# Performance work log

Measured on AMD Instinct MI355X. Metric: run time of the kernel, lower is better.

## Reference

```python
import jax, jax.numpy as jnp
import numpy as np

B, L, N = 16, 64, 1024
HAND_DIM, J, HID = 99, 21, 512
N_LAYERS, N_HEADS = 4, 8
DH = HID // N_HEADS
CAT = HAND_DIM + 2 * J * 3 + 2 * N  # 2273
PNAMES = ['fc_lw','fc_lb','fc_rw','fc_rb','out_lw','out_lb','out_rw','out_rb','Wqkv','bqkv','Wo','bo','W1','b1f','W2','b2f','ln1_g','ln1_b','ln2_g','ln2_b']

def sinusoidal_pe(n_pos, d):
    pos = np.arange(n_pos)[:, None].astype(np.float32)
    div = np.exp(np.arange(0, d, 2).astype(np.float32) * (-np.log(10000.0) / d))
    pe = np.zeros((n_pos, d), np.float32)
    pe[:, 0::2] = np.sin(pos * div)
    pe[:, 1::2] = np.cos(pos * div)
    return jnp.asarray(pe)

def rot6d_to_rotmat(x6):
    a1, a2 = x6[..., 0:3], x6[..., 3:6]
    b1 = a1 / jnp.linalg.norm(a1, axis=-1, keepdims=True)
    b2 = a2 - jnp.sum(b1 * a2, -1, keepdims=True) * b1
    b2 = b2 / jnp.linalg.norm(b2, axis=-1, keepdims=True)
    b3 = jnp.cross(b1, b2)
    return jnp.stack([b1, b2, b3], axis=-1)  # [..., 3, 3] (columns)

def layer_norm(x, g, b):
    mu = jnp.mean(x, -1, keepdims=True)
    var = jnp.mean((x - mu) ** 2, -1, keepdims=True)
    return (x - mu) * jax.lax.rsqrt(var + 1e-5) * g + b

def attention_map(joints, pc):
    # joints [B,L,J,3], pc [B,L,N,3]; squared dists via ||a||^2+||b||^2-2ab (no [B,L,J,N,3] diff tensor)
    d2 = (jnp.sum(joints ** 2, -1)[..., :, None] + jnp.sum(pc ** 2, -1)[..., None, :]
          - 2.0 * jnp.einsum('bljd,blnd->bljn', joints, pc))
    idx = jnp.argmin(d2, axis=-1)  # [B,L,J] nearest-point index
    idx3 = jnp.broadcast_to(idx[..., None], idx.shape + (3,))
    contact = jnp.take_along_axis(pc, idx3, axis=2)  # [B,L,J,3]
    return jnp.exp(-50.0 * (joints - contact) ** 2)

def mha(x, Wqkv, bqkv, Wo, bo):
    Bq, S, D = x.shape
    qkv = x @ Wqkv + bqkv
    q, k, v = jnp.split(qkv, 3, axis=-1)
    split = lambda t: t.reshape(Bq, S, N_HEADS, DH).transpose(0, 2, 1, 3)
    q, k, v = split(q), split(k), split(v)
    att = jax.nn.softmax(jnp.einsum('bhqd,bhkd->bhqk', q, k) * (1.0 / np.sqrt(DH)), axis=-1)
    o = jnp.einsum('bhqk,bhkd->bhqd', att, v).transpose(0, 2, 1, 3).reshape(Bq, S, D)
    return o @ Wo + bo

def forward(x_lhand, x_rhand, j_lhand, j_rhand, m_contact, x_obj, point_cloud, p):
    rotmat = rot6d_to_rotmat(x_obj[..., 3:9])  # [B,L,3,3]
    pc_t = jnp.einsum('btij,bkj->btki', rotmat, point_cloud) + x_obj[..., 0:3][:, :, None, :]
    att_l = attention_map(j_lhand, pc_t).reshape(B, L, -1)
    att_r = attention_map(j_rhand, pc_t).reshape(B, L, -1)
    mc = jnp.broadcast_to(m_contact.reshape(B, 1, N), (B, L, N))
    pcn = jnp.linalg.norm(pc_t, axis=-1)  # [B,L,N]
    xl = jnp.concatenate([x_lhand, j_lhand.reshape(B, L, -1), mc, pcn, att_l], -1)
    xr = jnp.concatenate([x_rhand, j_rhand.reshape(B, L, -1), mc, pcn, att_r], -1)
    xl = xl @ p['fc_lw'] + p['fc_lb']
    xr = xr @ p['fc_rw'] + p['fc_rb']
    x = jnp.stack([xl, xr], axis=2).reshape(B, 2 * L, HID)  # interleave agents per frame
    pe_frame = jnp.repeat(sinusoidal_pe(L, HID), 2, axis=0)  # frame-wise: pair shares position
    pe_agent = jnp.tile(sinusoidal_pe(2, HID), (L, 1))       # agent-wise: alternating 0/1
    x = x + pe_frame[None] + pe_agent[None]
    for i in range(N_LAYERS):
        h = layer_norm(x + mha(x, p['Wqkv'][i], p['bqkv'][i], p['Wo'][i], p['bo'][i]), p['ln1_g'][i], p['ln1_b'][i])
        ff = jax.nn.relu(h @ p['W1'][i] + p['b1f'][i]) @ p['W2'][i] + p['b2f'][i]
        x = layer_norm(h + ff, p['ln2_g'][i], p['ln2_b'][i])
    out_l = x[:, 0::2] @ p['out_lw'] + p['out_lb']
    out_r = x[:, 1::2] @ p['out_rw'] + p['out_rb']
    return out_l, out_r

def setup_inputs() -> dict:
    key = jax.random.key(0)
    ks = jax.random.split(key, 16)
    r = lambda i, shape, s=1.0: jax.random.normal(ks[i], shape, jnp.float32) * s
    return {
        'x_lhand': r(0, (B, L, HAND_DIM)),
        'x_rhand': r(1, (B, L, HAND_DIM)),
        'j_lhand': r(2, (B, L, J, 3)),
        'j_rhand': r(3, (B, L, J, 3)),
        'm_contact': jax.random.uniform(ks[4], (B, N, 1), jnp.float32),
        'x_obj': r(5, (B, L, 10)),
        'point_cloud': r(6, (B, N, 3)),
        'fc_lw': r(7, (CAT, HID), 0.02), 'fc_lb': jnp.zeros((HID,), jnp.float32),
        'fc_rw': r(8, (CAT, HID), 0.02), 'fc_rb': jnp.zeros((HID,), jnp.float32),
        'out_lw': r(9, (HID, HAND_DIM), 0.02), 'out_lb': jnp.zeros((HAND_DIM,), jnp.float32),
        'out_rw': r(10, (HID, HAND_DIM), 0.02), 'out_rb': jnp.zeros((HAND_DIM,), jnp.float32),
        'Wqkv': r(11, (N_LAYERS, HID, 3 * HID), 0.02), 'bqkv': jnp.zeros((N_LAYERS, 3 * HID), jnp.float32),
        'Wo': r(12, (N_LAYERS, HID, HID), 0.02), 'bo': jnp.zeros((N_LAYERS, HID), jnp.float32),
        'W1': r(13, (N_LAYERS, HID, 4 * HID), 0.02), 'b1f': jnp.zeros((N_LAYERS, 4 * HID), jnp.float32),
        'W2': r(14, (N_LAYERS, 4 * HID, HID), 0.02), 'b2f': jnp.zeros((N_LAYERS, HID), jnp.float32),
        'ln1_g': jnp.ones((N_LAYERS, HID), jnp.float32), 'ln1_b': jnp.zeros((N_LAYERS, HID), jnp.float32),
        'ln2_g': jnp.ones((N_LAYERS, HID), jnp.float32), 'ln2_b': jnp.zeros((N_LAYERS, HID), jnp.float32),
    }

def reference(x_lhand, x_rhand, j_lhand, j_rhand, m_contact, x_obj, point_cloud, fc_lw, fc_lb, fc_rw, fc_rb, out_lw, out_lb, out_rw, out_rb, Wqkv, bqkv, Wo, bo, W1, b1f, W2, b2f, ln1_g, ln1_b, ln2_g, ln2_b):
    p = dict(zip(PNAMES, (fc_lw, fc_lb, fc_rw, fc_rb, out_lw, out_lb, out_rw, out_rb, Wqkv, bqkv, Wo, bo, W1, b1f, W2, b2f, ln1_g, ln1_b, ln2_g, ln2_b)))
    return forward(x_lhand, x_rhand, j_lhand, j_rhand, m_contact, x_obj, point_cloud, p)
```

## Files before the change

### kernel.cpp

```cpp
#include <hip/hip_runtime.h>
#include <hip/hip_bf16.h>

typedef __hip_bfloat16 bf16;
typedef __attribute__((ext_vector_type(8))) short short8;
typedef __attribute__((ext_vector_type(4))) float floatx4;

#define B_    16
#define L_    64
#define N_    1024
#define HANDD 99
#define Jn    21
#define HID   512
#define NLAY  4
#define NHEAD 8
#define DHEAD 64
#define CATD  2273
#define CATP  2304
#define S_    128
#define T_    2048

#define F_X     16
#define F_QKV   1048592
#define F_TMP   6291472
#define F_H     7340048
#define WB_F    8388624
#define W_FCL   0
#define W_FCR   1179648
#define W_QKV   2359296
#define W_WO    5505024
#define W_W1    6553600
#define W_W2    10747904
#define U_CATL  14942208
#define U_CATR  17301504
#define U_XB    19660800
#define U_AOB   20709376
#define U_HB    21757952
#define W_OUT   22806528
#define U_FFB   U_CATL

static __device__ __forceinline__ float b2f(bf16 x) { return __bfloat162float(x); }
static __device__ __forceinline__ float ldin(const void* p, size_t i, int isf32) {
    return isf32 ? ((const float*)p)[i] : b2f(((const bf16*)p)[i]);
}
static __device__ __forceinline__ unsigned short f2bf(float f) {
    unsigned int u = __float_as_uint(f);
    unsigned int r = (u + 0x7fffu + ((u >> 16) & 1u)) >> 16;
    return (unsigned short)r;
}

__global__ __launch_bounds__(256) void detect_kernel(const void* mc, int* flag)
{
    __shared__ int sbad;
    int tid = threadIdx.x;
    if (tid == 0) sbad = 0;
    __syncthreads();
    int bad = 0;
    for (int i = tid; i < 16384; i += 256) {
        float v = b2f(((const bf16*)mc)[i]);
        if (!(v >= -0.02f && v <= 1.02f)) bad = 1;
    }
    if (bad) atomicOr(&sbad, 1);
    __syncthreads();
    if (tid == 0) flag[0] = sbad ? 1 : 0;
}

__global__ __launch_bounds__(256) void wtrans_kernel(
    const void* __restrict__ src, size_t src_layer, int K, int Nn, int NnBound,
    int Kpad, unsigned short* __restrict__ dst, size_t dst_layer,
    const int* __restrict__ dtf)
{
    int isf32 = dtf[0];
    __shared__ float tile[64][65];
    int lay = blockIdx.z;
    size_t soff = (size_t)lay * src_layer;
    size_t doff = (size_t)lay * dst_layer;
    int n0 = blockIdx.x * 64, k0 = blockIdx.y * 64;
    int a = threadIdx.x & 63, bq = threadIdx.x >> 6;
    for (int r = bq; r < 64; r += 4) {
        int k = k0 + r;
        int n = n0 + a;
        float v = (k < K && n < NnBound) ? ldin(src, soff + (size_t)k * Nn + n, isf32) : 0.f;
        tile[r][a] = v;
    }
    __syncthreads();
    for (int r = bq; r < 64; r += 4) {
        dst[doff + (size_t)(n0 + r) * Kpad + k0 + a] = f2bf(tile[a][r]);
    }
}

__global__ __launch_bounds__(256) void pctcat_kernel(
    const void* __restrict__ x_l, const void* __restrict__ j_l,
    const void* __restrict__ x_r, const void* __restrict__ j_r,
    const void* __restrict__ mc, const void* __restrict__ x_obj,
    const void* __restrict__ pc, unsigned short* __restrict__ cat_l,
    unsigned short* __restrict__ cat_r, const int* __restrict__ dtf)
{
    __shared__ float pcl[N_ * 3];
    __shared__ float pcnl[N_];
    int isf32 = dtf[0];
    int bl = blockIdx.x;
    int b  = bl >> 6;
    int tid = threadIdx.x;

    size_t xo = (size_t)bl * 10;
    float t0 = ldin(x_obj, xo+0, isf32), t1 = ldin(x_obj, xo+1, isf32), t2 = ldin(x_obj, xo+2, isf32);
    float a1x = ldin(x_obj, xo+3, isf32), a1y = ldin(x_obj, xo+4, isf32), a1z = ldin(x_obj, xo+5, isf32);
    float a2x = ldin(x_obj, xo+6, isf32), a2y = ldin(x_obj, xo+7, isf32), a2z = ldin(x_obj, xo+8, isf32);
    float n1 = sqrtf(a1x*a1x + a1y*a1y + a1z*a1z);
    float b1x = a1x / n1, b1y = a1y / n1, b1z = a1z / n1;
    float d = b1x*a2x + b1y*a2y + b1z*a2z;
    float c2x = a2x - d*b1x, c2y = a2y - d*b1y, c2z = a2z - d*b1z;
    float n2 = sqrtf(c2x*c2x + c2y*c2y + c2z*c2z);
    float b2x = c2x / n2, b2y = c2y / n2, b2z = c2z / n2;
    float b3x = b1y*b2z - b1z*b2y;
    float b3y = b1z*b2x - b1x*b2z;
    float b3z = b1x*b2y - b1y*b2x;

    size_t pcb = (size_t)b * N_ * 3;
    for (int n = tid; n < N_; n += 256) {
        float p0 = ldin(pc, pcb + n*3+0, isf32);
        float p1 = ldin(pc, pcb + n*3+1, isf32);
        float p2 = ldin(pc, pcb + n*3+2, isf32);
        float q0 = b1x*p0 + b2x*p1 + b3x*p2 + t0;
        float q1 = b1y*p0 + b2y*p1 + b3y*p2 + t1;
        float q2 = b1z*p0 + b2z*p1 + b3z*p2 + t2;
        pcl[n*3+0] = q0; pcl[n*3+1] = q1; pcl[n*3+2] = q2;
        pcnl[n] = q0*q0 + q1*q1 + q2*q2;
    }
    __syncthreads();

    #pragma unroll
    for (int hand = 0; hand < 2; hand++) {
        const void* xh = hand ? x_r : x_l;
        const void* jh = hand ? j_r : j_l;
        unsigned short* row = (hand ? cat_r : cat_l) + (size_t)bl * CATP;
        for (int c = tid; c < HANDD; c += 256)  row[c]        = f2bf(ldin(xh, (size_t)bl*HANDD + c, isf32));
        for (int c = tid; c < 63;    c += 256)  row[99 + c]   = f2bf(ldin(jh, (size_t)bl*63 + c, isf32));
        for (int c = tid; c < N_;    c += 256)  row[162 + c]  = f2bf(ldin(mc, (size_t)b*N_ + c, isf32));
        for (int c = tid; c < N_;    c += 256)  row[1186 + c] = f2bf(sqrtf(pcnl[c]));
        for (int c = CATD + tid; c < CATP; c += 256) row[c] = 0;
    }

    int wave = tid >> 6, lane = tid & 63;
    for (int t = wave; t < 2 * Jn; t += 4) {
        int hand = t / Jn, j = t - hand * Jn;
        const void* jh = hand ? j_r : j_l;
        unsigned short* row = (hand ? cat_r : cat_l) + (size_t)bl * CATP;
        float jx = ldin(jh, (size_t)bl*63 + j*3 + 0, isf32);
        float jy = ldin(jh, (size_t)bl*63 + j*3 + 1, isf32);
        float jz = ldin(jh, (size_t)bl*63 + j*3 + 2, isf32);
        float m2x = -2.f * jx, m2y = -2.f * jy, m2z = -2.f * jz;
        float best = 3.4e38f; int bidx = 0x7fffffff;
        for (int n = lane; n < N_; n += 64) {
            float p0 = pcl[n*3+0], p1 = pcl[n*3+1], p2 = pcl[n*3+2];
            float d2 = fmaf(m2x, p0, fmaf(m2y, p1, fmaf(m2z, p2, pcnl[n])));
            if (d2 < best) { best = d2; bidx = n; }
        }
        for (int off = 32; off; off >>= 1) {
            float ob = __shfl_down(best, off, 64);
            int   oi = __shfl_down(bidx, off, 64);
            if (ob < best || (ob == best && oi < bidx)) { best = ob; bidx = oi; }
        }
        bidx = __shfl(bidx, 0, 64);
        if (lane < 3) {
            float jc = (lane == 0) ? jx : ((lane == 1) ? jy : jz);
            float cc = pcl[bidx*3 + lane];
            float dd = jc - cc;
            row[2210 + j*3 + lane] = f2bf(expf(-50.f * dd * dd));
        }
    }
}

#define RSTR 68

__global__ __launch_bounds__(256) void gemm_ks(
    const unsigned short* __restrict__ Ab, const unsigned short* __restrict__ Ab2,
    int K,
    const unsigned short* __restrict__ Wt, size_t wtoff, size_t wtoff2, int halfgrid,
    int Nn,
    const void* __restrict__ bias, const void* __restrict__ bias2, size_t boff,
    const float* __restrict__ resid,
    float* __restrict__ Df, unsigned short* __restrict__ Db,
    int relu, int rowmap, int tilesN, const int* __restrict__ dtf)
{
    __shared__ float red[4][32 * RSTR];
    int blk = blockIdx.x;
    if (halfgrid && blk >= halfgrid) {
        blk -= halfgrid; Ab = Ab2; wtoff = wtoff2; bias = bias2; rowmap = 2;
    }
    int tid = threadIdx.x;
    int wave = tid >> 6, lane = tid & 63;
    int quad = lane >> 4, l16 = lane & 15;
    int tm = blk / tilesN, tn = blk - tm * tilesN;
    int row0 = tm << 6, col0 = tn << 6;
    int Ks = K >> 2;
    int ks0 = wave * Ks;

    const unsigned short* Ap = Ab + (size_t)(row0 + l16) * K + ks0 + quad * 8;
    const unsigned short* Bp = Wt + wtoff + (size_t)(col0 + l16) * K + ks0 + quad * 8;
    size_t astep = (size_t)16 * K;

    floatx4 acc[4][4];
    #pragma unroll
    for (int i = 0; i < 4; i++)
        #pragma unroll
        for (int j = 0; j < 4; j++)
            acc[i][j] = (floatx4){0.f, 0.f, 0.f, 0.f};

    for (int k = 0; k < Ks; k += 32) {
        short8 af[4], bf[4];
        #pragma unroll
        for (int i = 0; i < 4; i++) {
            af[i] = *(const short8*)(Ap + i * astep + k);
            bf[i] = *(const short8*)(Bp + i * astep + k);
        }
        #pragma unroll
        for (int mi = 0; mi < 4; mi++)
            #pragma unroll
            for (int ni = 0; ni < 4; ni++)
                acc[mi][ni] = __builtin_amdgcn_mfma_f32_16x16x32_bf16(
                    af[mi], bf[ni], acc[mi][ni], 0, 0, 0);
    }

    int isf32 = dtf[0];
    int cc = tid & 63;
    int c = col0 + cc;
    float bv;
    if (rowmap == 3)
        bv = (c < HANDD) ? ldin(bias, c, isf32)
           : ((c < 2 * HANDD) ? ldin(bias2, c - HANDD, isf32) : 0.f);
    else
        bv = bias ? ldin(bias, boff + c, isf32) : 0.f;
    float pe_div = 0.f, pa = 0.f;
    if (rowmap == 1 || rowmap == 2) {
        int ci = c & ~1;
        pe_div = expf((float)ci * (-logf(10000.f) / (float)HID));
        int hand = rowmap - 1;
        pa = (c & 1) ? cosf((float)hand * pe_div) : sinf((float)hand * pe_div);
    }
    int rbase = tid >> 6;

    #pragma unroll
    for (int s = 0; s < 2; s++) {
        #pragma unroll
        for (int mi2 = 0; mi2 < 2; mi2++) {
            int mi = s * 2 + mi2;
            #pragma unroll
            for (int ni = 0; ni < 4; ni++)
                #pragma unroll
                for (int reg = 0; reg < 4; reg++) {
                    int r = mi2 * 16 + quad * 4 + reg;
                    int col = ni * 16 + l16;
                    red[wave][r * RSTR + col] = acc[mi][ni][reg];
                }
        }
        __syncthreads();

        #pragma unroll
        for (int j = 0; j < 8; j++) {
            int rr = rbase + (j << 2);
            int idx = rr * RSTR + cc;
            float v = red[0][idx] + red[1][idx] + red[2][idx] + red[3][idx] + bv;
            int r = row0 + s * 32 + rr;
            if (resid) v += resid[(size_t)r * Nn + c];
            if (relu)  v = fmaxf(v, 0.f);
            if (rowmap == 3) {
                int hand = r & 1;
                int l = (r >> 1) & 63, bb = r >> 7;
                if (hand == 0 && c < HANDD) {
                    size_t oi = ((size_t)bb * 64 + l) * HANDD + c;
                    if (isf32) ((float*)Df)[oi] = v;
                    else       ((bf16*)Df)[oi]  = __float2bfloat16(v);
                } else if (hand == 1 && c >= HANDD && c < 2 * HANDD) {
                    size_t oi = (size_t)B_ * L_ * HANDD + ((size_t)bb * 64 + l) * HANDD + (c - HANDD);
                    if (isf32) ((float*)Df)[oi] = v;
                    else       ((bf16*)Df)[oi]  = __float2bfloat16(v);
                }
            } else {
                int orow = r;
                if (rowmap) {
                    int bb = r >> 6, ll = r & 63;
                    orow = bb * S_ + 2 * ll + (rowmap - 1);
                    float pf = (c & 1) ? cosf((float)ll * pe_div) : sinf((float)ll * pe_div);
                    v += pf + pa;
                }
                if (Df) Df[(size_t)orow * Nn + c] = v;
                if (Db) Db[(size_t)orow * Nn + c] = f2bf(v);
            }
        }
        if (s == 0) __syncthreads();
    }
}

#define VSTR 136

__global__ __launch_bounds__(128) void attn_mfma(
    const unsigned short* __restrict__ qkvb, unsigned short* __restrict__ aob)
{
    __shared__ unsigned short Vt[64 * VSTR];
    __shared__ unsigned short Pb[64 * VSTR];
    int bh = blockIdx.x;
    int b = bh >> 3, h = bh & 7;
    int rowhalf = blockIdx.y;
    int tid = threadIdx.x;
    int w = tid >> 6, lane = tid & 63;
    int quad = lane >> 4, l16 = lane & 15;
    size_t qbase = (size_t)(b * S_) * 1536 + h * DHEAD;

    for (int i = tid; i < S_ * DHEAD; i += 128) {
        int key = i >> 6, dcol = i & 63;
        Vt[dcol * VSTR + key] = qkvb[qbase + (size_t)key * 1536 + 1024 + dcol];
    }
    __syncthreads();

    int qrow0 = rowhalf * 64 + w * 32;
    short8 aQ[2][2];
    #pragma unroll
    for (int mt = 0; mt < 2; mt++)
        #pragma unroll
        for (int kc = 0; kc < 2; kc++)
            aQ[mt][kc] = *(const short8*)&qkvb[qbase + (size_t)(qrow0 + mt*16 + l16) * 1536 + kc*32 + quad*8];

    floatx4 sacc[2][8];
    #pragma unroll
    for (int mt = 0; mt < 2; mt++)
        #pragma unroll
        for (int nt = 0; nt < 8; nt++)
            sacc[mt][nt] = (floatx4){0.f, 0.f, 0.f, 0.f};

    #pragma unroll
    for (int nt = 0; nt < 8; nt++) {
        const unsigned short* kp = &qkvb[qbase + (size_t)(nt*16 + l16) * 1536 + 512 + quad*8];
        short8 bK0 = *(const short8*)kp;
        short8 bK1 = *(const short8*)(kp + 32);
        #pragma unroll
        for (int mt = 0; mt < 2; mt++) {
            sacc[mt][nt] = __builtin_amdgcn_mfma_f32_16x16x32_bf16(aQ[mt][0], bK0, sacc[mt][nt], 0, 0, 0);
            sacc[mt][nt] = __builtin_amdgcn_mfma_f32_16x16x32_bf16(aQ[mt][1], bK1, sacc[mt][nt], 0, 0, 0);
        }
    }

    #pragma unroll
    for (int mt = 0; mt < 2; mt++)
        #pragma unroll
        for (int reg = 0; reg < 4; reg++) {
            float v[8];
            float m = -3.4e38f;
            #pragma unroll
            for (int nt = 0; nt < 8; nt++) { v[nt] = sacc[mt][nt][reg] * 0.125f; m = fmaxf(m, v[nt]); }
            #pragma unroll
            for (int off = 1; off <= 8; off <<= 1) m = fmaxf(m, __shfl_xor(m, off, 64));
            float sum = 0.f;
            #pragma unroll
            for (int nt = 0; nt < 8; nt++) { v[nt] = expf(v[nt] - m); sum += v[nt]; }
            #pragma unroll
            for (int off = 1; off <= 8; off <<= 1) sum += __shfl_xor(sum, off, 64);
            float inv = 1.f / sum;
            int lr = w*32 + mt*16 + quad*4 + reg;
            #pragma unroll
            for (int nt = 0; nt < 8; nt++)
                Pb[lr * VSTR + nt*16 + l16] = f2bf(v[nt] * inv);
        }
    __syncthreads();

    #pragma unroll
    for (int mt = 0; mt < 2; mt++) {
        short8 aP[4];
        #pragma unroll
        for (int kt = 0; kt < 4; kt++)
            aP[kt] = *(const short8*)&Pb[(w*32 + mt*16 + l16) * VSTR + kt*32 + quad*8];
        #pragma unroll
        for (int nt = 0; nt < 4; nt++) {
            floatx4 o = (floatx4){0.f, 0.f, 0.f, 0.f};
            #pragma unroll
            for (int kt = 0; kt < 4; kt++) {
                short8 bV = *(const short8*)&Vt[(nt*16 + l16) * VSTR + kt*32 + quad*8];
                o = __builtin_amdgcn_mfma_f32_16x16x32_bf16(aP[kt], bV, o, 0, 0, 0);
            }
            #pragma unroll
            for (int reg = 0; reg < 4; reg++) {
                int qrow = qrow0 + mt*16 + quad*4 + reg;
                aob[(size_t)(b*S_ + qrow) * HID + h*DHEAD + nt*16 + l16] = f2bf(o[reg]);
            }
        }
    }
}

__global__ __launch_bounds__(256) void ln_kernel(
    const float* __restrict__ src, const void* __restrict__ g,
    const void* __restrict__ bb, size_t goff,
    float* __restrict__ dst, unsigned short* __restrict__ dstb,
    const int* __restrict__ dtf)
{
    int isf32 = dtf[0];
    int t = blockIdx.x;
    const float* x = src + (size_t)t * HID;
    int tid = threadIdx.x, lane = tid & 63, wave = tid >> 6;
    float v0 = x[tid], v1 = x[tid + 256];
    float s = v0 + v1;
    for (int off = 32; off; off >>= 1) s += __shfl_down(s, off, 64);
    __shared__ float wsum[4];
    if (lane == 0) wsum[wave] = s;
    __syncthreads();
    float mu = (wsum[0] + wsum[1] + wsum[2] + wsum[3]) * (1.f / 512.f);
    float d0 = v0 - mu, d1 = v1 - mu;
    float q = d0 * d0 + d1 * d1;
    for (int off = 32; off; off >>= 1) q += __shfl_down(q, off, 64);
    __syncthreads();
    if (lane == 0) wsum[wave] = q;
    __syncthreads();
    float var = (wsum[0] + wsum[1] + wsum[2] + wsum[3]) * (1.f / 512.f);
    float rstd = 1.f / sqrtf(var + 1e-5f);
    float y0 = d0 * rstd * ldin(g, goff + tid, isf32)       + ldin(bb, goff + tid, isf32);
    float y1 = d1 * rstd * ldin(g, goff + tid + 256, isf32) + ldin(bb, goff + tid + 256, isf32);
    if (dst) {
        dst[(size_t)t * HID + tid]       = y0;
        dst[(size_t)t * HID + tid + 256] = y1;
    }
    if (dstb) {
        dstb[(size_t)t * HID + tid]       = f2bf(y0);
        dstb[(size_t)t * HID + tid + 256] = f2bf(y1);
    }
}

extern "C" void kernel_launch(void* const* d_in, const int* in_sizes, int n_in,
                              void* d_out, int out_size, void* d_ws, size_t ws_size,
                              hipStream_t stream)
{
    const void* x_lhand = d_in[0];
    const void* x_rhand = d_in[1];
    const void* j_lhand = d_in[2];
    const void* j_rhand = d_in[3];
    const void* m_contact = d_in[4];
    const void* x_obj = d_in[5];
    const void* point_cloud = d_in[6];
    const void* fc_lw = d_in[7];
    const void* fc_lb = d_in[8];
    const void* fc_rw = d_in[9];
    const void* fc_rb = d_in[10];
    const void* out_lw = d_in[11];
    const void* out_lb = d_in[12];
    const void* out_rw = d_in[13];
    const void* out_rb = d_in[14];
    const void* Wqkv = d_in[15];
    const void* bqkv = d_in[16];
    const void* Wo   = d_in[17];
    const void* bo   = d_in[18];
    const void* W1   = d_in[19];
    const void* b1f  = d_in[20];
    const void* W2   = d_in[21];
    const void* b2fp = d_in[22];
    const void* ln1g = d_in[23];
    const void* ln1b = d_in[24];
    const void* ln2g = d_in[25];
    const void* ln2b = d_in[26];

    float* ws = (float*)d_ws;
    int* dtf = (int*)d_ws;
    float* x     = ws + F_X;
    float* tmp   = ws + F_TMP;
    float* h     = ws + F_H;
    unsigned short* qkvb = (unsigned short*)(ws + F_QKV);
    unsigned short* wb   = (unsigned short*)(ws + WB_F);
    unsigned short* catl = wb + U_CATL;
    unsigned short* catr = wb + U_CATR;
    unsigned short* xb   = wb + U_XB;
    unsigned short* aob  = wb + U_AOB;
    unsigned short* hb   = wb + U_HB;
    unsigned short* ffb  = wb + U_FFB;

    detect_kernel<<<1, 256, 0, stream>>>(m_contact, dtf);

    wtrans_kernel<<<dim3(8, 36, 1), 256, 0, stream>>>(fc_lw, 0, CATD, HID, HID, CATP, wb + W_FCL, 0, dtf);
    wtrans_kernel<<<dim3(8, 36, 1), 256, 0, stream>>>(fc_rw, 0, CATD, HID, HID, CATP, wb + W_FCR, 0, dtf);
    wtrans_kernel<<<dim3(24, 8, NLAY), 256, 0, stream>>>(Wqkv, (size_t)HID*1536, HID, 1536, 1536, HID, wb + W_QKV, (size_t)1536*HID, dtf);
    wtrans_kernel<<<dim3(8, 8, NLAY), 256, 0, stream>>>(Wo, (size_t)HID*HID, HID, HID, HID, HID, wb + W_WO, (size_t)HID*HID, dtf);
    wtrans_kernel<<<dim3(32, 8, NLAY), 256, 0, stream>>>(W1, (size_t)HID*2048, HID, 2048, 2048, HID, wb + W_W1, (size_t)2048*HID, dtf);
    wtrans_kernel<<<dim3(8, 32, NLAY), 256, 0, stream>>>(W2, (size_t)2048*HID, 2048, HID, HID, 2048, wb + W_W2, (size_t)HID*2048, dtf);
    wtrans_kernel<<<dim3(2, 8, 1), 256, 0, stream>>>(out_lw, 0, HID, HANDD, HANDD, HID, wb + W_OUT, 0, dtf);
    wtrans_kernel<<<dim3(2, 8, 1), 256, 0, stream>>>(out_rw, 0, HID, HANDD, HANDD, HID, wb + W_OUT + (size_t)HANDD * HID, 0, dtf);

    pctcat_kernel<<<B_ * L_, 256, 0, stream>>>(
        x_lhand, j_lhand, x_rhand, j_rhand, m_contact, x_obj, point_cloud,
        catl, catr, dtf);

    gemm_ks<<<256, 256, 0, stream>>>(catl, catr, CATP, wb, W_FCL, W_FCR, 128, HID,
                                     fc_lb, fc_rb, 0, nullptr, x, xb, 0, 1, 8, dtf);

    for (int i = 0; i < NLAY; i++) {
        size_t oWq = (size_t)W_QKV + (size_t)i * 1536 * HID, obq = (size_t)i * 1536;
        size_t oWo = (size_t)W_WO + (size_t)i * HID * HID,   obo = (size_t)i * HID;
        size_t oW1 = (size_t)W_W1 + (size_t)i * 2048 * HID,  ob1 = (size_t)i * 2048;
        size_t oW2 = (size_t)W_W2 + (size_t)i * HID * 2048,  ob2 = (size_t)i * HID;
        size_t oln = (size_t)i * HID;

        gemm_ks<<<768, 256, 0, stream>>>(xb, nullptr, HID, wb, oWq, 0, 0, 1536,
                                         bqkv, nullptr, obq, nullptr, nullptr, qkvb, 0, 0, 24, dtf);

        attn_mfma<<<dim3(B_ * NHEAD, 2), 128, 0, stream>>>(qkvb, aob);

        gemm_ks<<<256, 256, 0, stream>>>(aob, nullptr, HID, wb, oWo, 0, 0, HID,
                                         bo, nullptr, obo, x, tmp, nullptr, 0, 0, 8, dtf);
        ln_kernel<<<T_, 256, 0, stream>>>(tmp, ln1g, ln1b, oln, h, hb, dtf);

        gemm_ks<<<1024, 256, 0, stream>>>(hb, nullptr, HID, wb, oW1, 0, 0, 2048,
                                          b1f, nullptr, ob1, nullptr, nullptr, ffb, 1, 0, 32, dtf);
        gemm_ks<<<256, 256, 0, stream>>>(ffb, nullptr, 2048, wb, oW2, 0, 0, HID,
                                         b2fp, nullptr, ob2, h, tmp, nullptr, 0, 0, 8, dtf);
        ln_kernel<<<T_, 256, 0, stream>>>(tmp, ln2g, ln2b, oln, x, xb, dtf);
    }

    gemm_ks<<<128, 256, 0, stream>>>(xb, nullptr, HID, wb, W_OUT, 0, 0, 256,
                                     out_lb, out_rb, 0, nullptr, (float*)d_out, nullptr, 0, 3, 4, dtf);
}
```

Measured before the change: 717.7 us.

## Fuse LayerNorm into GEMM prologues/epilogues via atomic row statistics

```diff
diff --git a/kernel.cpp b/kernel.cpp
--- a/kernel.cpp
+++ b/kernel.cpp
@@ -19,11 +19,15 @@
 #define S_    128
 #define T_    2048
 
-#define F_X     16
-#define F_QKV   1048592
-#define F_TMP   6291472
-#define F_H     7340048
-#define WB_F    8388624
+#define F_X      16
+#define F_QKV    1048592
+#define F_STATS1 4000000
+#define F_S2A    4004096
+#define F_S2B    4008192
+#define F_LNP    4012288
+#define F_TMP    6291472
+#define F_T2     7340048
+#define WB_F     8388624
 #define W_FCL   0
 #define W_FCR   1179648
 #define W_QKV   2359296
@@ -34,9 +38,11 @@
 #define U_CATR  17301504
 #define U_XB    19660800
 #define U_AOB   20709376
-#define U_HB    21757952
 #define W_OUT   22806528
 #define U_FFB   U_CATL
+
+#define RSTR 68
+#define VSTR 136
 
 static __device__ __forceinline__ float b2f(bf16 x) { return __bfloat162float(x); }
 static __device__ __forceinline__ float ldin(const void* p, size_t i, int isf32) {
@@ -64,27 +70,75 @@
     if (tid == 0) flag[0] = sbad ? 1 : 0;
 }
 
-__global__ __launch_bounds__(256) void wtrans_kernel(
-    const void* __restrict__ src, size_t src_layer, int K, int Nn, int NnBound,
-    int Kpad, unsigned short* __restrict__ dst, size_t dst_layer,
-    const int* __restrict__ dtf)
+struct WtP {
+    const void *fc_lw, *fc_rw, *Wqkv, *Wo, *W1, *W2, *out_lw, *out_rw;
+    const void *ln1g, *ln1b, *ln2g, *ln2b;
+    unsigned short* wb; float* lnp;
+    const int* dtf;
+};
+
+__global__ __launch_bounds__(256) void wtrans_all(WtP P)
 {
-    int isf32 = dtf[0];
+    int isf32 = P.dtf[0];
+    int u = blockIdx.x;
+    if (u == 3680) {
+        for (int idx = threadIdx.x; idx < 8192; idx += 256) {
+            int layer = idx >> 11, rem = idx & 2047;
+            int which = rem >> 9, pos = rem & 511;
+            const void* src = (which == 0) ? P.ln1g : (which == 1) ? P.ln1b
+                            : (which == 2) ? P.ln2g : P.ln2b;
+            P.lnp[idx] = ldin(src, (size_t)layer * 512 + pos, isf32);
+        }
+        unsigned short* wz = P.wb + W_OUT + (size_t)(2 * HANDD) * HID;
+        for (int idx = threadIdx.x; idx < (256 - 2 * HANDD) * HID; idx += 256)
+            wz[idx] = 0;
+        return;
+    }
     __shared__ float tile[64][65];
-    int lay = blockIdx.z;
-    size_t soff = (size_t)lay * src_layer;
-    size_t doff = (size_t)lay * dst_layer;
-    int n0 = blockIdx.x * 64, k0 = blockIdx.y * 64;
+    const void* src; unsigned short* dst;
+    int K, Nn, NnB, Kpad, gx; size_t soff = 0, doff = 0;
+    if (u < 576) {
+        int hh = u >= 288; if (hh) u -= 288;
+        src = hh ? P.fc_rw : P.fc_lw; dst = P.wb + (hh ? W_FCR : W_FCL);
+        K = CATD; Nn = HID; NnB = HID; Kpad = CATP; gx = 8;
+    } else if (u < 1344) {
+        int r = u - 576; int z = r / 192; u = r % 192;
+        src = P.Wqkv; soff = (size_t)z * HID * 1536;
+        dst = P.wb + W_QKV; doff = (size_t)z * 1536 * HID;
+        K = HID; Nn = 1536; NnB = 1536; Kpad = HID; gx = 24;
+    } else if (u < 1600) {
+        int r = u - 1344; int z = r / 64; u = r % 64;
+        src = P.Wo; soff = (size_t)z * HID * HID;
+        dst = P.wb + W_WO; doff = (size_t)z * HID * HID;
+        K = HID; Nn = HID; NnB = HID; Kpad = HID; gx = 8;
+    } else if (u < 2624) {
+        int r = u - 1600; int z = r / 256; u = r % 256;
+        src = P.W1; soff = (size_t)z * HID * 2048;
+        dst = P.wb + W_W1; doff = (size_t)z * 2048 * HID;
+        K = HID; Nn = 2048; NnB = 2048; Kpad = HID; gx = 32;
+    } else if (u < 3648) {
+        int r = u - 2624; int z = r / 256; u = r % 256;
+        src = P.W2; soff = (size_t)z * 2048 * HID;
+        dst = P.wb + W_W2; doff = (size_t)z * HID * 2048;
+        K = 2048; Nn = HID; NnB = HID; Kpad = 2048; gx = 8;
+    } else {
+        int r = u - 3648; int hh = r >= 16; if (hh) r -= 16;
+        src = hh ? P.out_rw : P.out_lw;
+        dst = P.wb + W_OUT + (hh ? (size_t)HANDD * HID : 0);
+        K = HID; Nn = HANDD; NnB = HANDD; Kpad = HID; gx = 2; u = r;
+    }
+    int n0 = (u % gx) * 64, k0 = (u / gx) * 64;
     int a = threadIdx.x & 63, bq = threadIdx.x >> 6;
     for (int r = bq; r < 64; r += 4) {
-        int k = k0 + r;
-        int n = n0 + a;
-        float v = (k < K && n < NnBound) ? ldin(src, soff + (size_t)k * Nn + n, isf32) : 0.f;
+        int k = k0 + r, n = n0 + a;
+        float v = (k < K && n < NnB) ? ldin(src, soff + (size_t)k * Nn + n, isf32) : 0.f;
         tile[r][a] = v;
     }
     __syncthreads();
     for (int r = bq; r < 64; r += 4) {
-        dst[doff + (size_t)(n0 + r) * Kpad + k0 + a] = f2bf(tile[a][r]);
+        int n = n0 + r;
+        if (n < NnB)
+            dst[doff + (size_t)n * Kpad + k0 + a] = f2bf(tile[a][r]);
     }
 }
 
@@ -171,24 +225,29 @@
     }
 }
 
-#define RSTR 68
-
+template<int NORMA>
 __global__ __launch_bounds__(256) void gemm_ks(
     const unsigned short* __restrict__ Ab, const unsigned short* __restrict__ Ab2,
+    const float* __restrict__ Af, const float* __restrict__ astats,
+    const float* __restrict__ ag, const float* __restrict__ abeta,
     int K,
     const unsigned short* __restrict__ Wt, size_t wtoff, size_t wtoff2, int halfgrid,
     int Nn,
     const void* __restrict__ bias, const void* __restrict__ bias2, size_t boff,
-    const float* __restrict__ resid,
+    int residmode, const float* __restrict__ rsrc,
+    const float* __restrict__ rstats, const float* __restrict__ rg, const float* __restrict__ rb,
+    float* __restrict__ ostats, float* __restrict__ zbuf,
     float* __restrict__ Df, unsigned short* __restrict__ Db,
     int relu, int rowmap, int tilesN, const int* __restrict__ dtf)
 {
     __shared__ float red[4][32 * RSTR];
+    int tid = threadIdx.x;
+    if (zbuf && blockIdx.x < 16) zbuf[blockIdx.x * 256 + tid] = 0.f;
+
     int blk = blockIdx.x;
     if (halfgrid && blk >= halfgrid) {
         blk -= halfgrid; Ab = Ab2; wtoff = wtoff2; bias = bias2; rowmap = 2;
     }
-    int tid = threadIdx.x;
     int wave = tid >> 6, lane = tid & 63;
     int quad = lane >> 4, l16 = lane & 15;
     int tm = blk / tilesN, tn = blk - tm * tilesN;
@@ -196,7 +255,6 @@
     int Ks = K >> 2;
     int ks0 = wave * Ks;
 
-    const unsigned short* Ap = Ab + (size_t)(row0 + l16) * K + ks0 + quad * 8;
     const unsigned short* Bp = Wt + wtoff + (size_t)(col0 + l16) * K + ks0 + quad * 8;
     size_t astep = (size_t)16 * K;
 
@@ -207,19 +265,60 @@
         for (int j = 0; j < 4; j++)
             acc[i][j] = (floatx4){0.f, 0.f, 0.f, 0.f};
 
-    for (int k = 0; k < Ks; k += 32) {
-        short8 af[4], bf[4];
+    if constexpr (NORMA == 0) {
+        const unsigned short* Ap = Ab + (size_t)(row0 + l16) * K + ks0 + quad * 8;
+        for (int k = 0; k < Ks; k += 32) {
+            short8 af[4], bf[4];
+            #pragma unroll
+            for (int i = 0; i < 4; i++) {
+                af[i] = *(const short8*)(Ap + i * astep + k);
+                bf[i] = *(const short8*)(Bp + i * astep + k);
+            }
+            #pragma unroll
+            for (int mi = 0; mi < 4; mi++)
+                #pragma unroll
+                for (int ni = 0; ni < 4; ni++)
+                    acc[mi][ni] = __builtin_amdgcn_mfma_f32_16x16x32_bf16(
+                        af[mi], bf[ni], acc[mi][ni], 0, 0, 0);
+        }
+    } else {
+        const float* Ap4[4]; float s_[4], t_[4];
         #pragma unroll
         for (int i = 0; i < 4; i++) {
-            af[i] = *(const short8*)(Ap + i * astep + k);
-            bf[i] = *(const short8*)(Bp + i * astep + k);
-        }
-        #pragma unroll
-        for (int mi = 0; mi < 4; mi++)
-            #pragma unroll
-            for (int ni = 0; ni < 4; ni++)
-                acc[mi][ni] = __builtin_amdgcn_mfma_f32_16x16x32_bf16(
-                    af[mi], bf[ni], acc[mi][ni], 0, 0, 0);
+            int r = row0 + l16 + i * 16;
+            Ap4[i] = Af + (size_t)r * K + ks0 + quad * 8;
+            float sm = astats[r*2+0], sq = astats[r*2+1];
+            float mu = sm * (1.f / 512.f);
+            float var = fmaxf(sq * (1.f / 512.f) - mu * mu, 0.f);
+            float rstd = rsqrtf(var + 1e-5f);
+            s_[i] = rstd; t_[i] = -mu * rstd;
+        }
+        const float* gp = ag + ks0 + quad * 8;
+        const float* bp = abeta + ks0 + quad * 8;
+        for (int k = 0; k < Ks; k += 32) {
+            floatx4 g0 = *(const floatx4*)(gp + k), g1v = *(const floatx4*)(gp + k + 4);
+            floatx4 b0 = *(const floatx4*)(bp + k), b1v = *(const floatx4*)(bp + k + 4);
+            short8 af[4], bf[4];
+            #pragma unroll
+            for (int i = 0; i < 4; i++) {
+                floatx4 v0 = *(const floatx4*)(Ap4[i] + k);
+                floatx4 v1 = *(const floatx4*)(Ap4[i] + k + 4);
+                #pragma unroll
+                for (int e = 0; e < 4; e++) {
+                    float y0 = fmaf(fmaf(v0[e], s_[i], t_[i]), g0[e], b0[e]);
+                    float y1 = fmaf(fmaf(v1[e], s_[i], t_[i]), g1v[e], b1v[e]);
+                    af[i][e]     = (short)f2bf(y0);
+                    af[i][e + 4] = (short)f2bf(y1);
+                }
+                bf[i] = *(const short8*)(Bp + i * astep + k);
+            }
+            #pragma unroll
+            for (int mi = 0; mi < 4; mi++)
+                #pragma unroll
+                for (int ni = 0; ni < 4; ni++)
+                    acc[mi][ni] = __builtin_amdgcn_mfma_f32_16x16x32_bf16(
+                        af[mi], bf[ni], acc[mi][ni], 0, 0, 0);
+        }
     }
 
     int isf32 = dtf[0];
@@ -238,6 +337,8 @@
         int hand = rowmap - 1;
         pa = (c & 1) ? cosf((float)hand * pe_div) : sinf((float)hand * pe_div);
     }
+    float rg_c = 0.f, rb_c = 0.f;
+    if (residmode == 2) { rg_c = rg[c]; rb_c = rb[c]; }
     int rbase = tid >> 6;
 
     #pragma unroll
@@ -262,8 +363,30 @@
             int idx = rr * RSTR + cc;
             float v = red[0][idx] + red[1][idx] + red[2][idx] + red[3][idx] + bv;
             int r = row0 + s * 32 + rr;
-            if (resid) v += resid[(size_t)r * Nn + c];
-            if (relu)  v = fmaxf(v, 0.f);
+            if (residmode == 1) {
+                v += rsrc[(size_t)r * 512 + c];
+            } else if (residmode == 2) {
+                float sm = rstats[r*2+0], sq = rstats[r*2+1];
+                float mu = sm * (1.f / 512.f);
+                float var = fmaxf(sq * (1.f / 512.f) - mu * mu, 0.f);
+                float rstd = rsqrtf(var + 1e-5f);
+                v += fmaf((rsrc[(size_t)r * 512 + c] - mu) * rstd, rg_c, rb_c);
+            }
+            if (relu) v = fmaxf(v, 0.f);
+
+            if (ostats) {
+                float sv = v, sq2 = v * v;
+                #pragma unroll
+                for (int off = 32; off; off >>= 1) {
+                    sv  += __shfl_xor(sv,  off, 64);
+                    sq2 += __shfl_xor(sq2, off, 64);
+                }
+                if (lane == 0) {
+                    atomicAdd(&ostats[r*2+0], sv);
+                    atomicAdd(&ostats[r*2+1], sq2);
+                }
+            }
+
             if (rowmap == 3) {
                 int hand = r & 1;
                 int l = (r >> 1) & 63, bb = r >> 7;
@@ -278,7 +401,7 @@
                 }
             } else {
                 int orow = r;
-                if (rowmap) {
+                if (rowmap == 1 || rowmap == 2) {
                     int bb = r >> 6, ll = r & 63;
                     orow = bb * S_ + 2 * ll + (rowmap - 1);
                     float pf = (c & 1) ? cosf((float)ll * pe_div) : sinf((float)ll * pe_div);
@@ -292,17 +415,18 @@
     }
 }
 
-#define VSTR 136
-
 __global__ __launch_bounds__(128) void attn_mfma(
-    const unsigned short* __restrict__ qkvb, unsigned short* __restrict__ aob)
+    const unsigned short* __restrict__ qkvb, unsigned short* __restrict__ aob,
+    float* __restrict__ zbuf)
 {
     __shared__ unsigned short Vt[64 * VSTR];
     __shared__ unsigned short Pb[64 * VSTR];
+    int tid = threadIdx.x;
+    if (zbuf && blockIdx.y == 0 && blockIdx.x < 32) zbuf[blockIdx.x * 128 + tid] = 0.f;
+
     int bh = blockIdx.x;
     int b = bh >> 3, h = bh & 7;
     int rowhalf = blockIdx.y;
-    int tid = threadIdx.x;
     int w = tid >> 6, lane = tid & 63;
     int quad = lane >> 4, l16 = lane & 15;
     size_t qbase = (size_t)(b * S_) * 1536 + h * DHEAD;
@@ -383,43 +507,6 @@
                 aob[(size_t)(b*S_ + qrow) * HID + h*DHEAD + nt*16 + l16] = f2bf(o[reg]);
             }
         }
-    }
-}
-
-__global__ __launch_bounds__(256) void ln_kernel(
-    const float* __restrict__ src, const void* __restrict__ g,
-    const void* __restrict__ bb, size_t goff,
-    float* __restrict__ dst, unsigned short* __restrict__ dstb,
-    const int* __restrict__ dtf)
-{
-    int isf32 = dtf[0];
-    int t = blockIdx.x;
-    const float* x = src + (size_t)t * HID;
-    int tid = threadIdx.x, lane = tid & 63, wave = tid >> 6;
-    float v0 = x[tid], v1 = x[tid + 256];
-    float s = v0 + v1;
-    for (int off = 32; off; off >>= 1) s += __shfl_down(s, off, 64);
-    __shared__ float wsum[4];
-    if (lane == 0) wsum[wave] = s;
-    __syncthreads();
-    float mu = (wsum[0] + wsum[1] + wsum[2] + wsum[3]) * (1.f / 512.f);
-    float d0 = v0 - mu, d1 = v1 - mu;
-    float q = d0 * d0 + d1 * d1;
-    for (int off = 32; off; off >>= 1) q += __shfl_down(q, off, 64);
-    __syncthreads();
-    if (lane == 0) wsum[wave] = q;
-    __syncthreads();
-    float var = (wsum[0] + wsum[1] + wsum[2] + wsum[3]) * (1.f / 512.f);
-    float rstd = 1.f / sqrtf(var + 1e-5f);
-    float y0 = d0 * rstd * ldin(g, goff + tid, isf32)       + ldin(bb, goff + tid, isf32);
-    float y1 = d1 * rstd * ldin(g, goff + tid + 256, isf32) + ldin(bb, goff + tid + 256, isf32);
-    if (dst) {
-        dst[(size_t)t * HID + tid]       = y0;
-        dst[(size_t)t * HID + tid + 256] = y1;
-    }
-    if (dstb) {
-        dstb[(size_t)t * HID + tid]       = f2bf(y0);
-        dstb[(size_t)t * HID + tid + 256] = f2bf(y1);
     }
 }
 
@@ -457,59 +544,90 @@
 
     float* ws = (float*)d_ws;
     int* dtf = (int*)d_ws;
-    float* x     = ws + F_X;
-    float* tmp   = ws + F_TMP;
-    float* h     = ws + F_H;
+    float* x       = ws + F_X;
+    float* tmp     = ws + F_TMP;
+    float* tmp2    = ws + F_T2;
+    float* ln1st   = ws + F_STATS1;
+    float* s2[2]   = { ws + F_S2A, ws + F_S2B };
+    float* lnp     = ws + F_LNP;
     unsigned short* qkvb = (unsigned short*)(ws + F_QKV);
     unsigned short* wb   = (unsigned short*)(ws + WB_F);
     unsigned short* catl = wb + U_CATL;
     unsigned short* catr = wb + U_CATR;
     unsigned short* xb   = wb + U_XB;
     unsigned short* aob  = wb + U_AOB;
-    unsigned short* hb   = wb + U_HB;
     unsigned short* ffb  = wb + U_FFB;
 
     detect_kernel<<<1, 256, 0, stream>>>(m_contact, dtf);
 
-    wtrans_kernel<<<dim3(8, 36, 1), 256, 0, stream>>>(fc_lw, 0, CATD, HID, HID, CATP, wb + W_FCL, 0, dtf);
-    wtrans_kernel<<<dim3(8, 36, 1), 256, 0, stream>>>(fc_rw, 0, CATD, HID, HID, CATP, wb + W_FCR, 0, dtf);
-    wtrans_kernel<<<dim3(24, 8, NLAY), 256, 0, stream>>>(Wqkv, (size_t)HID*1536, HID, 1536, 1536, HID, wb + W_QKV, (size_t)1536*HID, dtf);
-    wtrans_kernel<<<dim3(8, 8, NLAY), 256, 0, stream>>>(Wo, (size_t)HID*HID, HID, HID, HID, HID, wb + W_WO, (size_t)HID*HID, dtf);
-    wtrans_kernel<<<dim3(32, 8, NLAY), 256, 0, stream>>>(W1, (size_t)HID*2048, HID, 2048, 2048, HID, wb + W_W1, (size_t)2048*HID, dtf);
-    wtrans_kernel<<<dim3(8, 32, NLAY), 256, 0, stream>>>(W2, (size_t)2048*HID, 2048, HID, HID, 2048, wb + W_W2, (size_t)HID*2048, dtf);
-    wtrans_kernel<<<dim3(2, 8, 1), 256, 0, stream>>>(out_lw, 0, HID, HANDD, HANDD, HID, wb + W_OUT, 0, dtf);
-    wtrans_kernel<<<dim3(2, 8, 1), 256, 0, stream>>>(out_rw, 0, HID, HANDD, HANDD, HID, wb + W_OUT + (size_t)HANDD * HID, 0, dtf);
+    WtP wp;
+    wp.fc_lw = fc_lw; wp.fc_rw = fc_rw; wp.Wqkv = Wqkv; wp.Wo = Wo;
+    wp.W1 = W1; wp.W2 = W2; wp.out_lw = out_lw; wp.out_rw = out_rw;
+    wp.ln1g = ln1g; wp.ln1b = ln1b; wp.ln2g = ln2g; wp.ln2b = ln2b;
+    wp.wb = wb; wp.lnp = lnp; wp.dtf = dtf;
+    wtrans_all<<<3681, 256, 0, stream>>>(wp);
 
     pctcat_kernel<<<B_ * L_, 256, 0, stream>>>(
         x_lhand, j_lhand, x_rhand, j_rhand, m_contact, x_obj, point_cloud,
         catl, catr, dtf);
 
-    gemm_ks<<<256, 256, 0, stream>>>(catl, catr, CATP, wb, W_FCL, W_FCR, 128, HID,
-                                     fc_lb, fc_rb, 0, nullptr, x, xb, 0, 1, 8, dtf);
+    gemm_ks<0><<<256, 256, 0, stream>>>(
+        catl, catr, nullptr, nullptr, nullptr, nullptr, CATP,
+        wb, W_FCL, W_FCR, 128, HID, fc_lb, fc_rb, 0,
+        0, nullptr, nullptr, nullptr, nullptr, nullptr, nullptr,
+        x, xb, 0, 1, 8, dtf);
 
     for (int i = 0; i < NLAY; i++) {
         size_t oWq = (size_t)W_QKV + (size_t)i * 1536 * HID, obq = (size_t)i * 1536;
         size_t oWo = (size_t)W_WO + (size_t)i * HID * HID,   obo = (size_t)i * HID;
         size_t oW1 = (size_t)W_W1 + (size_t)i * 2048 * HID,  ob1 = (size_t)i * 2048;
         size_t oW2 = (size_t)W_W2 + (size_t)i * HID * 2048,  ob2 = (size_t)i * HID;
-        size_t oln = (size_t)i * HID;
-
-        gemm_ks<<<768, 256, 0, stream>>>(xb, nullptr, HID, wb, oWq, 0, 0, 1536,
-                                         bqkv, nullptr, obq, nullptr, nullptr, qkvb, 0, 0, 24, dtf);
-
-        attn_mfma<<<dim3(B_ * NHEAD, 2), 128, 0, stream>>>(qkvb, aob);
-
-        gemm_ks<<<256, 256, 0, stream>>>(aob, nullptr, HID, wb, oWo, 0, 0, HID,
-                                         bo, nullptr, obo, x, tmp, nullptr, 0, 0, 8, dtf);
-        ln_kernel<<<T_, 256, 0, stream>>>(tmp, ln1g, ln1b, oln, h, hb, dtf);
-
-        gemm_ks<<<1024, 256, 0, stream>>>(hb, nullptr, HID, wb, oW1, 0, 0, 2048,
-                                          b1f, nullptr, ob1, nullptr, nullptr, ffb, 1, 0, 32, dtf);
-        gemm_ks<<<256, 256, 0, stream>>>(ffb, nullptr, 2048, wb, oW2, 0, 0, HID,
-                                         b2fp, nullptr, ob2, h, tmp, nullptr, 0, 0, 8, dtf);
-        ln_kernel<<<T_, 256, 0, stream>>>(tmp, ln2g, ln2b, oln, x, xb, dtf);
-    }
-
-    gemm_ks<<<128, 256, 0, stream>>>(xb, nullptr, HID, wb, W_OUT, 0, 0, 256,
-                                     out_lb, out_rb, 0, nullptr, (float*)d_out, nullptr, 0, 3, 4, dtf);
-}
+        float* s2prev = s2[(i + 1) & 1];
+        float* s2cur  = s2[i & 1];
+        float* gprev2 = lnp + (size_t)(i ? (i - 1) : 0) * 2048 + 1024;
+        float* bprev2 = lnp + (size_t)(i ? (i - 1) : 0) * 2048 + 1536;
+        float* g1 = lnp + (size_t)i * 2048;
+        float* b1 = lnp + (size_t)i * 2048 + 512;
+
+        if (i == 0)
+            gemm_ks<0><<<768, 256, 0, stream>>>(
+                xb, nullptr, nullptr, nullptr, nullptr, nullptr, HID,
+                wb, oWq, 0, 0, 1536, bqkv, nullptr, obq,
+                0, nullptr, nullptr, nullptr, nullptr, nullptr, ln1st,
+                nullptr, qkvb, 0, 0, 24, dtf);
+        else
+            gemm_ks<1><<<768, 256, 0, stream>>>(
+                nullptr, nullptr, tmp2, s2prev, gprev2, bprev2, HID,
+                wb, oWq, 0, 0, 1536, bqkv, nullptr, obq,
+                0, nullptr, nullptr, nullptr, nullptr, nullptr, ln1st,
+                nullptr, qkvb, 0, 0, 24, dtf);
+
+        attn_mfma<<<dim3(B_ * NHEAD, 2), 128, 0, stream>>>(qkvb, aob, s2cur);
+
+        gemm_ks<0><<<256, 256, 0, stream>>>(
+            aob, nullptr, nullptr, nullptr, nullptr, nullptr, HID,
+            wb, oWo, 0, 0, HID, bo, nullptr, obo,
+            (i == 0) ? 1 : 2, (i == 0) ? x : tmp2,
+            (i == 0) ? nullptr : s2prev, (i == 0) ? nullptr : gprev2,
+            (i == 0) ? nullptr : bprev2,
+            ln1st, nullptr, tmp, nullptr, 0, 0, 8, dtf);
+
+        gemm_ks<1><<<1024, 256, 0, stream>>>(
+            nullptr, nullptr, tmp, ln1st, g1, b1, HID,
+            wb, oW1, 0, 0, 2048, b1f, nullptr, ob1,
+            0, nullptr, nullptr, nullptr, nullptr, nullptr, nullptr,
+            nullptr, ffb, 1, 0, 32, dtf);
+
+        gemm_ks<0><<<256, 256, 0, stream>>>(
+            ffb, nullptr, nullptr, nullptr, nullptr, nullptr, 2048,
+            wb, oW2, 0, 0, HID, b2fp, nullptr, ob2,
+            2, tmp, ln1st, g1, b1,
+            s2cur, nullptr, tmp2, nullptr, 0, 0, 8, dtf);
+    }
+
+    gemm_ks<1><<<128, 256, 0, stream>>>(
+        nullptr, nullptr, tmp2, s2[1], lnp + 3*2048 + 1024, lnp + 3*2048 + 1536, HID,
+        wb, W_OUT, 0, 0, 256, out_lb, out_rb, 0,
+        0, nullptr, nullptr, nullptr, nullptr, nullptr, nullptr,
+        (float*)d_out, nullptr, 0, 3, 4, dtf);
+}
```

Measured after the change: 899.5 us. 1.25x slower.

## Merge weight transposes and point-cloud concat prep into one launch

Applied to the files above, without the earlier changes.

```diff
diff --git a/kernel.cpp b/kernel.cpp
--- a/kernel.cpp
+++ b/kernel.cpp
@@ -38,6 +38,12 @@
 #define W_OUT   22806528
 #define U_FFB   U_CATL
 
+#define RSTR 68
+#define VSTR 136
+
+#define PC_UNITS 2048
+#define NW_UNITS 3680
+
 static __device__ __forceinline__ float b2f(bf16 x) { return __bfloat162float(x); }
 static __device__ __forceinline__ float ldin(const void* p, size_t i, int isf32) {
     return isf32 ? ((const float*)p)[i] : b2f(((const bf16*)p)[i]);
@@ -64,48 +70,25 @@
     if (tid == 0) flag[0] = sbad ? 1 : 0;
 }
 
-__global__ __launch_bounds__(256) void wtrans_kernel(
-    const void* __restrict__ src, size_t src_layer, int K, int Nn, int NnBound,
-    int Kpad, unsigned short* __restrict__ dst, size_t dst_layer,
-    const int* __restrict__ dtf)
-{
-    int isf32 = dtf[0];
-    __shared__ float tile[64][65];
-    int lay = blockIdx.z;
-    size_t soff = (size_t)lay * src_layer;
-    size_t doff = (size_t)lay * dst_layer;
-    int n0 = blockIdx.x * 64, k0 = blockIdx.y * 64;
-    int a = threadIdx.x & 63, bq = threadIdx.x >> 6;
-    for (int r = bq; r < 64; r += 4) {
-        int k = k0 + r;
-        int n = n0 + a;
-        float v = (k < K && n < NnBound) ? ldin(src, soff + (size_t)k * Nn + n, isf32) : 0.f;
-        tile[r][a] = v;
-    }
-    __syncthreads();
-    for (int r = bq; r < 64; r += 4) {
-        dst[doff + (size_t)(n0 + r) * Kpad + k0 + a] = f2bf(tile[a][r]);
-    }
-}
-
-__global__ __launch_bounds__(256) void pctcat_kernel(
-    const void* __restrict__ x_l, const void* __restrict__ j_l,
-    const void* __restrict__ x_r, const void* __restrict__ j_r,
-    const void* __restrict__ mc, const void* __restrict__ x_obj,
-    const void* __restrict__ pc, unsigned short* __restrict__ cat_l,
-    unsigned short* __restrict__ cat_r, const int* __restrict__ dtf)
-{
-    __shared__ float pcl[N_ * 3];
-    __shared__ float pcnl[N_];
-    int isf32 = dtf[0];
-    int bl = blockIdx.x;
-    int b  = bl >> 6;
+struct PrepP {
+    const void *x_l, *x_r, *j_l, *j_r, *mc, *x_obj, *pc;
+    const void *fc_lw, *fc_rw, *Wqkv, *Wo, *W1, *W2, *out_lw, *out_rw;
+    unsigned short *wb, *catl, *catr;
+    const int* dtf;
+};
+
+static __device__ void pctcat_half(int bl, int hand, const PrepP& P, int isf32,
+                                   char* smemc)
+{
+    float* pcl  = (float*)smemc;
+    float* pcnl = pcl + N_ * 3;
+    int b = bl >> 6;
     int tid = threadIdx.x;
 
     size_t xo = (size_t)bl * 10;
-    float t0 = ldin(x_obj, xo+0, isf32), t1 = ldin(x_obj, xo+1, isf32), t2 = ldin(x_obj, xo+2, isf32);
-    float a1x = ldin(x_obj, xo+3, isf32), a1y = ldin(x_obj, xo+4, isf32), a1z = ldin(x_obj, xo+5, isf32);
-    float a2x = ldin(x_obj, xo+6, isf32), a2y = ldin(x_obj, xo+7, isf32), a2z = ldin(x_obj, xo+8, isf32);
+    float t0 = ldin(P.x_obj, xo+0, isf32), t1 = ldin(P.x_obj, xo+1, isf32), t2 = ldin(P.x_obj, xo+2, isf32);
+    float a1x = ldin(P.x_obj, xo+3, isf32), a1y = ldin(P.x_obj, xo+4, isf32), a1z = ldin(P.x_obj, xo+5, isf32);
+    float a2x = ldin(P.x_obj, xo+6, isf32), a2y = ldin(P.x_obj, xo+7, isf32), a2z = ldin(P.x_obj, xo+8, isf32);
     float n1 = sqrtf(a1x*a1x + a1y*a1y + a1z*a1z);
     float b1x = a1x / n1, b1y = a1y / n1, b1z = a1z / n1;
     float d = b1x*a2x + b1y*a2y + b1z*a2z;
@@ -118,9 +101,9 @@
 
     size_t pcb = (size_t)b * N_ * 3;
     for (int n = tid; n < N_; n += 256) {
-        float p0 = ldin(pc, pcb + n*3+0, isf32);
-        float p1 = ldin(pc, pcb + n*3+1, isf32);
-        float p2 = ldin(pc, pcb + n*3+2, isf32);
+        float p0 = ldin(P.pc, pcb + n*3+0, isf32);
+        float p1 = ldin(P.pc, pcb + n*3+1, isf32);
+        float p2 = ldin(P.pc, pcb + n*3+2, isf32);
         float q0 = b1x*p0 + b2x*p1 + b3x*p2 + t0;
         float q1 = b1y*p0 + b2y*p1 + b3y*p2 + t1;
         float q2 = b1z*p0 + b2z*p1 + b3z*p2 + t2;
@@ -129,23 +112,17 @@
     }
     __syncthreads();
 
-    #pragma unroll
-    for (int hand = 0; hand < 2; hand++) {
-        const void* xh = hand ? x_r : x_l;
-        const void* jh = hand ? j_r : j_l;
-        unsigned short* row = (hand ? cat_r : cat_l) + (size_t)bl * CATP;
-        for (int c = tid; c < HANDD; c += 256)  row[c]        = f2bf(ldin(xh, (size_t)bl*HANDD + c, isf32));
-        for (int c = tid; c < 63;    c += 256)  row[99 + c]   = f2bf(ldin(jh, (size_t)bl*63 + c, isf32));
-        for (int c = tid; c < N_;    c += 256)  row[162 + c]  = f2bf(ldin(mc, (size_t)b*N_ + c, isf32));
-        for (int c = tid; c < N_;    c += 256)  row[1186 + c] = f2bf(sqrtf(pcnl[c]));
-        for (int c = CATD + tid; c < CATP; c += 256) row[c] = 0;
-    }
+    const void* xh = hand ? P.x_r : P.x_l;
+    const void* jh = hand ? P.j_r : P.j_l;
+    unsigned short* row = (hand ? P.catr : P.catl) + (size_t)bl * CATP;
+    for (int c = tid; c < HANDD; c += 256)  row[c]        = f2bf(ldin(xh, (size_t)bl*HANDD + c, isf32));
+    for (int c = tid; c < 63;    c += 256)  row[99 + c]   = f2bf(ldin(jh, (size_t)bl*63 + c, isf32));
+    for (int c = tid; c < N_;    c += 256)  row[162 + c]  = f2bf(ldin(P.mc, (size_t)b*N_ + c, isf32));
+    for (int c = tid; c < N_;    c += 256)  row[1186 + c] = f2bf(sqrtf(pcnl[c]));
+    for (int c = CATD + tid; c < CATP; c += 256) row[c] = 0;
 
     int wave = tid >> 6, lane = tid & 63;
-    for (int t = wave; t < 2 * Jn; t += 4) {
-        int hand = t / Jn, j = t - hand * Jn;
-        const void* jh = hand ? j_r : j_l;
-        unsigned short* row = (hand ? cat_r : cat_l) + (size_t)bl * CATP;
+    for (int j = wave; j < Jn; j += 4) {
         float jx = ldin(jh, (size_t)bl*63 + j*3 + 0, isf32);
         float jy = ldin(jh, (size_t)bl*63 + j*3 + 1, isf32);
         float jz = ldin(jh, (size_t)bl*63 + j*3 + 2, isf32);
@@ -171,7 +148,71 @@
     }
 }
 
-#define RSTR 68
+__global__ __launch_bounds__(256) void prep_all(PrepP P)
+{
+    __shared__ __attribute__((aligned(16))) char smem[16640];
+    int isf32 = P.dtf[0];
+    int u = blockIdx.x;
+
+    if (u < PC_UNITS) {
+        pctcat_half(u >> 1, u & 1, P, isf32, smem);
+        return;
+    }
+    u -= PC_UNITS;
+    if (u == NW_UNITS) {
+        unsigned short* wz = P.wb + W_OUT + (size_t)(2 * HANDD) * HID;
+        for (int idx = threadIdx.x; idx < (256 - 2 * HANDD) * HID; idx += 256)
+            wz[idx] = 0;
+        return;
+    }
+
+    float (*tile)[65] = (float(*)[65])smem;
+    const void* src; unsigned short* dst;
+    int K, Nn, NnB, Kpad, gx; size_t soff = 0, doff = 0;
+    if (u < 576) {
+        int hh = u >= 288; if (hh) u -= 288;
+        src = hh ? P.fc_rw : P.fc_lw; dst = P.wb + (hh ? W_FCR : W_FCL);
+        K = CATD; Nn = HID; NnB = HID; Kpad = CATP; gx = 8;
+    } else if (u < 1344) {
+        int r = u - 576; int z = r / 192; u = r % 192;
+        src = P.Wqkv; soff = (size_t)z * HID * 1536;
+        dst = P.wb + W_QKV; doff = (size_t)z * 1536 * HID;
+        K = HID; Nn = 1536; NnB = 1536; Kpad = HID; gx = 24;
+    } else if (u < 1600) {
+        int r = u - 1344; int z = r / 64; u = r % 64;
+        src = P.Wo; soff = (size_t)z * HID * HID;
+        dst = P.wb + W_WO; doff = (size_t)z * HID * HID;
+        K = HID; Nn = HID; NnB = HID; Kpad = HID; gx = 8;
+    } else if (u < 2624) {
+        int r = u - 1600; int z = r / 256; u = r % 256;
+        src = P.W1; soff = (size_t)z * HID * 2048;
+        dst = P.wb + W_W1; doff = (size_t)z * 2048 * HID;
+        K = HID; Nn = 2048; NnB = 2048; Kpad = HID; gx = 32;
+    } else if (u < 3648) {
+        int r = u - 2624; int z = r / 256; u = r % 256;
+        src = P.W2; soff = (size_t)z * 2048 * HID;
+        dst = P.wb + W_W2; doff = (size_t)z * HID * 2048;
+        K = 2048; Nn = HID; NnB = HID; Kpad = 2048; gx = 8;
+    } else {
+        int r = u - 3648; int hh = r >= 16; if (hh) r -= 16;
+        src = hh ? P.out_rw : P.out_lw;
+        dst = P.wb + W_OUT + (hh ? (size_t)HANDD * HID : 0);
+        K = HID; Nn = HANDD; NnB = HANDD; Kpad = HID; gx = 2; u = r;
+    }
+    int n0 = (u % gx) * 64, k0 = (u / gx) * 64;
+    int a = threadIdx.x & 63, bq = threadIdx.x >> 6;
+    for (int r = bq; r < 64; r += 4) {
+        int k = k0 + r, n = n0 + a;
+        float v = (k < K && n < NnB) ? ldin(src, soff + (size_t)k * Nn + n, isf32) : 0.f;
+        tile[r][a] = v;
+    }
+    __syncthreads();
+    for (int r = bq; r < 64; r += 4) {
+        int n = n0 + r;
+        if (n < NnB)
+            dst[doff + (size_t)n * Kpad + k0 + a] = f2bf(tile[a][r]);
+    }
+}
 
 __global__ __launch_bounds__(256) void gemm_ks(
     const unsigned short* __restrict__ Ab, const unsigned short* __restrict__ Ab2,
@@ -292,8 +333,6 @@
     }
 }
 
-#define VSTR 136
-
 __global__ __launch_bounds__(128) void attn_mfma(
     const unsigned short* __restrict__ qkvb, unsigned short* __restrict__ aob)
 {
@@ -471,18 +510,13 @@
 
     detect_kernel<<<1, 256, 0, stream>>>(m_contact, dtf);
 
-    wtrans_kernel<<<dim3(8, 36, 1), 256, 0, stream>>>(fc_lw, 0, CATD, HID, HID, CATP, wb + W_FCL, 0, dtf);
-    wtrans_kernel<<<dim3(8, 36, 1), 256, 0, stream>>>(fc_rw, 0, CATD, HID, HID, CATP, wb + W_FCR, 0, dtf);
-    wtrans_kernel<<<dim3(24, 8, NLAY), 256, 0, stream>>>(Wqkv, (size_t)HID*1536, HID, 1536, 1536, HID, wb + W_QKV, (size_t)1536*HID, dtf);
-    wtrans_kernel<<<dim3(8, 8, NLAY), 256, 0, stream>>>(Wo, (size_t)HID*HID, HID, HID, HID, HID, wb + W_WO, (size_t)HID*HID, dtf);
-    wtrans_kernel<<<dim3(32, 8, NLAY), 256, 0, stream>>>(W1, (size_t)HID*2048, HID, 2048, 2048, HID, wb + W_W1, (size_t)2048*HID, dtf);
-    wtrans_kernel<<<dim3(8, 32, NLAY), 256, 0, stream>>>(W2, (size_t)2048*HID, 2048, HID, HID, 2048, wb + W_W2, (size_t)HID*2048, dtf);
-    wtrans_kernel<<<dim3(2, 8, 1), 256, 0, stream>>>(out_lw, 0, HID, HANDD, HANDD, HID, wb + W_OUT, 0, dtf);
-    wtrans_kernel<<<dim3(2, 8, 1), 256, 0, stream>>>(out_rw, 0, HID, HANDD, HANDD, HID, wb + W_OUT + (size_t)HANDD * HID, 0, dtf);
-
-    pctcat_kernel<<<B_ * L_, 256, 0, stream>>>(
-        x_lhand, j_lhand, x_rhand, j_rhand, m_contact, x_obj, point_cloud,
-        catl, catr, dtf);
+    PrepP pp;
+    pp.x_l = x_lhand; pp.x_r = x_rhand; pp.j_l = j_lhand; pp.j_r = j_rhand;
+    pp.mc = m_contact; pp.x_obj = x_obj; pp.pc = point_cloud;
+    pp.fc_lw = fc_lw; pp.fc_rw = fc_rw; pp.Wqkv = Wqkv; pp.Wo = Wo;
+    pp.W1 = W1; pp.W2 = W2; pp.out_lw = out_lw; pp.out_rw = out_rw;
+    pp.wb = wb; pp.catl = catl; pp.catr = catr; pp.dtf = dtf;
+    prep_all<<<PC_UNITS + NW_UNITS + 1, 256, 0, stream>>>(pp);
 
     gemm_ks<<<256, 256, 0, stream>>>(catl, catr, CATP, wb, W_FCL, W_FCR, 128, HID,
                                      fc_lb, fc_rb, 0, nullptr, x, xb, 0, 1, 8, dtf);
```

After: 648.1 us. 1.11x faster.
